# Kernel tuning notes

Hardware: AMD Instinct MI355X
Metric: run time of the kernel (lower is better)

## Reference

```python
import jax, jax.numpy as jnp
import numpy as np

HID = 4096; H = 128; P = 64; N = 128; G = 8; K = 4; CH = 128
INTER = H * P                      # 8192
CONV_DIM = INTER + 2 * G * N       # 10240
PROJ = INTER + CONV_DIM + H        # 18560
EPS = 1e-5


def segsum(x):
    # stable segment-sum: out[..., i, j] = sum_{j < k <= i} x[..., k]; -inf above diagonal
    T = x.shape[-1]
    xe = jnp.repeat(x[..., None], T, axis=-1)          # [..., i, j] = x[..., i]
    strict = jnp.tril(jnp.ones((T, T), bool), -1)
    s = jnp.cumsum(jnp.where(strict, xe, 0.0), axis=-2)
    keep = jnp.tril(jnp.ones((T, T), bool), 0)
    return jnp.where(keep, s, -jnp.inf)


def setup_inputs() -> dict:
    key = jax.random.key(0)
    ks = jax.random.split(key, 6)
    b, L = 2, 2048
    hidden_states = jax.random.normal(ks[0], (b, L, HID), jnp.float32)
    in_proj_w = jax.random.normal(ks[1], (PROJ, HID), jnp.float32) * (HID ** -0.5)
    conv_w = jax.random.normal(ks[2], (CONV_DIM, 1, K), jnp.float32) * 0.2
    conv_b = jax.random.normal(ks[3], (CONV_DIM,), jnp.float32) * 0.02
    dt_bias = jnp.ones((H,), jnp.float32)
    A_log = jnp.log(jnp.arange(1, H + 1, dtype=jnp.float32))
    D = jnp.ones((H,), jnp.float32)
    norm_weight = jnp.ones((INTER,), jnp.float32)
    out_proj_w = jax.random.normal(ks[4], (HID, INTER), jnp.float32) * (INTER ** -0.5)
    return dict(hidden_states=hidden_states, in_proj_w=in_proj_w, conv_w=conv_w, conv_b=conv_b,
                dt_bias=dt_bias, A_log=A_log, D=D, norm_weight=norm_weight, out_proj_w=out_proj_w)


def _mamba2(hidden_states, in_proj_w, conv_w, conv_b, dt_bias, A_log, D, norm_weight, out_proj_w):
    b, L, _ = hidden_states.shape
    nchunk = L // CH  # seq_len chosen to be a multiple of chunk_size (pad_size = 0)

    # in_proj and split into gate | conv path (x,B,C) | dt
    proj = hidden_states @ in_proj_w.T
    gate, hBC, dt = jnp.split(proj, [INTER, INTER + CONV_DIM], axis=-1)

    # causal depthwise conv1d (padding k-1, truncate) + SiLU
    xp = jnp.pad(hBC.transpose(0, 2, 1), ((0, 0), (0, 0), (K - 1, 0)))
    xc = jax.lax.conv_general_dilated(xp, conv_w, (1,), 'VALID',
                                      feature_group_count=CONV_DIM,
                                      dimension_numbers=('NCW', 'OIW', 'NCW'))
    hBC = jax.nn.silu((xc + conv_b[None, :, None]).transpose(0, 2, 1))
    hs, Bx, Cx = jnp.split(hBC, [INTER, INTER + G * N], axis=-1)

    A = -jnp.exp(A_log)                      # [H]
    dt = jax.nn.softplus(dt + dt_bias)       # time_step_limit = (0, inf) -> clamp is no-op

    hs = hs.reshape(b, L, H, P)
    rep = H // G
    Bm = jnp.tile(Bx.reshape(b, L, G, N), (1, 1, rep, 1))   # matches torch .repeat
    Cm = jnp.tile(Cx.reshape(b, L, G, N), (1, 1, rep, 1))

    D_res = D[None, None, :, None] * hs      # [b,L,H,P]

    # discretize and chunk
    X = (hs * dt[..., None]).reshape(b, nchunk, CH, H, P)
    A_dt = (A[None, None, :] * dt).reshape(b, nchunk, CH, H).transpose(0, 3, 1, 2)  # [b,H,c,l]
    Bc = Bm.reshape(b, nchunk, CH, H, N)
    Cc = Cm.reshape(b, nchunk, CH, H, N)
    A_cs = jnp.cumsum(A_dt, axis=-1)

    # 1. intra-chunk (diagonal blocks)
    Lmat = jnp.exp(segsum(A_dt))                              # [b,H,c,l,s]
    Gm = jnp.einsum('bclhn,bcshn->bclsh', Cc, Bc)
    M = Gm * Lmat.transpose(0, 2, 3, 4, 1)                    # [b,c,l,s,H]
    Y_diag = jnp.einsum('bclsh,bcshp->bclhp', M, X)

    # 2. per-chunk states
    decay_states = jnp.exp(A_cs[..., -1:] - A_cs)             # [b,H,c,l]
    B_decay = Bc * decay_states.transpose(0, 2, 3, 1)[..., None]
    states = jnp.einsum('bclhn,bclhp->bchpn', B_decay, X)     # [b,c,H,P,N]

    # 3. inter-chunk recurrence
    states = jnp.concatenate([jnp.zeros_like(states[:, :1]), states], axis=1)
    A_last = jnp.pad(A_cs[..., -1], ((0, 0), (0, 0), (1, 0)))  # [b,H,c+1]
    decay_chunk = jnp.exp(segsum(A_last)).transpose(0, 3, 2, 1)  # [b,c+1,c+1,H]
    new_states = jnp.einsum('bzjh,bzhpn->bjhpn', decay_chunk, states)
    prev_states = new_states[:, :-1]                           # [b,c,H,P,N]

    # 4. state -> output
    sdo = jnp.exp(A_cs).transpose(0, 2, 3, 1)                  # [b,c,l,H]
    Y_off = jnp.einsum('bclhn,bchpn->bclhp', Cc, prev_states) * sdo[..., None]

    y = (Y_diag + Y_off).reshape(b, L, H, P) + D_res
    scan_out = y.reshape(b, L, INTER)

    # gated group RMSNorm (norm_before_gate=False: gate first, then group-RMS)
    xg = scan_out * jax.nn.silu(gate)
    xr = xg.reshape(b, L, G, INTER // G)
    xr = xr * jax.lax.rsqrt(jnp.mean(xr * xr, axis=-1, keepdims=True) + EPS)
    normed = xr.reshape(b, L, INTER) * norm_weight

    return normed @ out_proj_w.T


def reference(hidden_states, in_proj_w, conv_w, conv_b, dt_bias, A_log, D, norm_weight, out_proj_w):
    return _mamba2(hidden_states, in_proj_w, conv_w, conv_b, dt_bias, A_log, D, norm_weight, out_proj_w)
```

## Files before the change

kernel.cpp:

```cpp
#include <hip/hip_runtime.h>

#define NH 128
#define PD 64
#define NSD 128
#define NG 8
#define CHK 128
#define HIDD 4096
#define INTER_D 8192
#define CONV_D 10240
#define PROJ_D 18560
#define SEQ 2048
#define ROWS 4096
#define NCH 16

typedef __attribute__((ext_vector_type(8))) short bf16x8;
typedef __attribute__((ext_vector_type(4))) float f32x4;

__device__ __forceinline__ unsigned short f2bf(float f) {
  unsigned int u = __float_as_uint(f);
  u += 0x7FFF + ((u >> 16) & 1);
  return (unsigned short)(u >> 16);
}
__device__ __forceinline__ float bf2f(unsigned short s) {
  return __uint_as_float(((unsigned int)s) << 16);
}

__device__ __forceinline__ void gld16(const unsigned short* g, unsigned short* l) {
  __builtin_amdgcn_global_load_lds(
      (__attribute__((address_space(1))) const void*)g,
      (__attribute__((address_space(3))) void*)l, 16, 0, 0);
}

#define BAR() __builtin_amdgcn_s_barrier()
#define SCHED() __builtin_amdgcn_sched_barrier(0)
#define VMCNT(n) asm volatile("s_waitcnt vmcnt(" #n ")" ::: "memory")

__device__ __forceinline__ bf16x8 ldsfrag(const unsigned short* slot, int row, int kslot) {
  int byte = row * 128 + (((kslot ^ (row & 7)) << 4));
  return *(const bf16x8*)((const char*)slot + byte);
}

__global__ __launch_bounds__(256) void cvt_all_kernel(const float* __restrict__ hs,
                                                      const float* __restrict__ w1,
                                                      const float* __restrict__ w2,
                                                      unsigned short* __restrict__ hsb,
                                                      unsigned short* __restrict__ w1b,
                                                      unsigned short* __restrict__ w2b) {
  int bid = blockIdx.x;
  const float* in;
  unsigned short* out;
  size_t base;
  if (bid < 16384) {
    in = hs; out = hsb; base = (size_t)bid * 1024;
  } else if (bid < 16384 + 74240) {
    in = w1; out = w1b; base = (size_t)(bid - 16384) * 1024;
  } else {
    in = w2; out = w2b; base = (size_t)(bid - 16384 - 74240) * 1024;
  }
  size_t i = base + (size_t)threadIdx.x * 4;
  float4 f = *(const float4*)(in + i);
  ushort4 o;
  o.x = f2bf(f.x); o.y = f2bf(f.y); o.z = f2bf(f.z); o.w = f2bf(f.w);
  *(ushort4*)(out + i) = o;
}

template <int OUT_BF16>
__global__ __launch_bounds__(512, 2) void gemm256(const unsigned short* __restrict__ A,
                                                  const unsigned short* __restrict__ B,
                                                  unsigned short* __restrict__ outb,
                                                  float* __restrict__ outf,
                                                  int Nreal, int Ks, int Kl, int koff) {
  __shared__ unsigned short lds[8][8192];
  int tid = threadIdx.x, l = tid & 63, w = tid >> 6;
  int wm = w >> 2, wn = w & 3;
  int il = l & 15, fog = l >> 4;
  int bid = blockIdx.x;
  int xcd = bid & 7, local = bid >> 3;
  int mt = xcd * 2 + (local & 1), nt = local >> 1;
  const unsigned short* Abase = A + (size_t)mt * 256 * Ks + koff;
  const unsigned short* Bbase = B + (size_t)nt * 256 * Ks + koff;
  int NT = Kl >> 6;

  f32x4 acc[2][2][4][2];
#pragma unroll
  for (int a = 0; a < 2; ++a)
#pragma unroll
    for (int b = 0; b < 2; ++b)
#pragma unroll
      for (int m = 0; m < 4; ++m)
#pragma unroll
        for (int n = 0; n < 2; ++n) acc[a][b][m][n] = (f32x4){0.f, 0.f, 0.f, 0.f};

  auto STG = [&](int tt, int ty) {
    int tc = tt < NT ? tt : NT - 1;
    const unsigned short* g = ((ty & 1) ? Bbase : Abase) + (size_t)((ty >> 1) * 128) * Ks + tc * 64;
    unsigned short* sp = (unsigned short*)lds[(tt & 1) * 4 + ty];
#pragma unroll
    for (int j = 0; j < 2; ++j) {
      int row = (j * 8 + w) * 8 + (l >> 3);
      int scol = ((l & 7) ^ (row & 7)) * 8;
      gld16(g + (size_t)row * Ks + scol, sp + (j * 8 + w) * 512);
    }
  };

#define LDA(SLOT)                                          \
  _Pragma("unroll") for (int mi = 0; mi < 4; ++mi)         \
  _Pragma("unroll") for (int kk = 0; kk < 2; ++kk)         \
      av[mi][kk] = ldsfrag(SLOT, wm * 64 + mi * 16 + il, kk * 4 + fog);
#define LDB(QN, SLOT)                                      \
  _Pragma("unroll") for (int ni = 0; ni < 2; ++ni)         \
  _Pragma("unroll") for (int kk = 0; kk < 2; ++kk)         \
      bv[QN][ni][kk] = ldsfrag(SLOT, wn * 32 + ni * 16 + il, kk * 4 + fog);
#define MFMA_PH(QM, QN)                                    \
  _Pragma("unroll") for (int mi = 0; mi < 4; ++mi)         \
  _Pragma("unroll") for (int ni = 0; ni < 2; ++ni)         \
  _Pragma("unroll") for (int kk = 0; kk < 2; ++kk)         \
      acc[QM][QN][mi][ni] = __builtin_amdgcn_mfma_f32_16x16x32_bf16( \
          av[mi][kk], bv[QN][ni][kk], acc[QM][QN][mi][ni], 0, 0, 0);

  STG(0, 0); STG(0, 1); STG(0, 3); STG(0, 2);
  VMCNT(2);
  BAR(); SCHED();

  for (int t = 0; t < NT; ++t) {
    const unsigned short* sA0 = lds[(t & 1) * 4 + 0];
    const unsigned short* sB0 = lds[(t & 1) * 4 + 1];
    const unsigned short* sA1 = lds[(t & 1) * 4 + 2];
    const unsigned short* sB1 = lds[(t & 1) * 4 + 3];
    bf16x8 av[4][2], bv[2][2][2];
    LDA(sA0); LDB(0, sB0); LDB(1, sB1);
    STG(t + 1, 0); STG(t + 1, 1);
    BAR();
    __builtin_amdgcn_s_setprio(1);
    MFMA_PH(0, 0);
    __builtin_amdgcn_s_setprio(0);
    VMCNT(4);
    BAR(); SCHED();
    STG(t + 1, 3);
    __builtin_amdgcn_s_setprio(1);
    MFMA_PH(0, 1);
    __builtin_amdgcn_s_setprio(0);
    BAR();
    LDA(sA1);
    STG(t + 1, 2);
    BAR();
    __builtin_amdgcn_s_setprio(1);
    MFMA_PH(1, 0);
    __builtin_amdgcn_s_setprio(0);
    BAR();
    __builtin_amdgcn_s_setprio(1);
    MFMA_PH(1, 1);
    __builtin_amdgcn_s_setprio(0);
    VMCNT(2);
    BAR(); SCHED();
  }
  VMCNT(0);

  int rl = (l >> 4) * 4;
#pragma unroll
  for (int qm = 0; qm < 2; ++qm)
#pragma unroll
    for (int qn = 0; qn < 2; ++qn)
#pragma unroll
      for (int mi = 0; mi < 4; ++mi)
#pragma unroll
        for (int ni = 0; ni < 2; ++ni) {
          int grow = mt * 256 + qm * 128 + wm * 64 + mi * 16 + rl;
          int gcol = nt * 256 + qn * 128 + wn * 32 + ni * 16 + il;
          if (!OUT_BF16 || gcol < Nreal) {
#pragma unroll
            for (int r = 0; r < 4; ++r) {
              float v = acc[qm][qn][mi][ni][r];
              if (OUT_BF16)
                outb[(size_t)(grow + r) * Nreal + gcol] = f2bf(v);
              else
                outf[(size_t)(grow + r) * Nreal + gcol] = v;
            }
          }
        }
#undef LDA
#undef LDB
#undef MFMA_PH
}

__global__ __launch_bounds__(256) void dtsa_kernel(const unsigned short* __restrict__ proj,
                                                   const float* __restrict__ dt_bias,
                                                   float* __restrict__ dtg) {
  int idx = blockIdx.x * 256 + threadIdx.x;
  int row = idx >> 7, h = idx & 127;
  float x = bf2f(proj[(size_t)row * PROJ_D + (PROJ_D - NH) + h]) + dt_bias[h];
  float d = (x > 20.f) ? x : log1pf(expf(x));
  dtg[(size_t)row * NH + h] = d;
}

__global__ __launch_bounds__(128) void dtsb_kernel(const float* __restrict__ dtg,
                                                   const float* __restrict__ A_log,
                                                   float* __restrict__ acsg) {
  int bc = blockIdx.x;
  int h = threadIdx.x;
  int b = bc >> 4, c = bc & 15;
  float A = -__expf(A_log[h]);
  float cum = 0.f;
  int row0 = b * SEQ + c * CHK;
#pragma unroll 8
  for (int ll = 0; ll < CHK; ++ll) {
    cum += A * dtg[(size_t)(row0 + ll) * NH + h];
    acsg[(((size_t)bc * NH) + h) * CHK + ll] = cum;
  }
}

__global__ __launch_bounds__(256) void conv_kernel(const unsigned short* __restrict__ proj,
                                                   const float* __restrict__ cw,
                                                   const float* __restrict__ cb,
                                                   unsigned short* __restrict__ xbc) {
  int ch0 = (blockIdx.x * 256 + threadIdx.x) * 8;
  int row = blockIdx.y;
  int b = row >> 11, ll = row & 2047;
  float4 cwv[8];
#pragma unroll
  for (int e = 0; e < 8; ++e) cwv[e] = *(const float4*)(cw + (ch0 + e) * 4);
  float acc[8];
#pragma unroll
  for (int e = 0; e < 8; ++e) acc[e] = cb[ch0 + e];
#pragma unroll
  for (int k = 0; k < 4; ++k) {
    int l2 = ll - 3 + k;
    if (l2 >= 0) {
      bf16x8 v = *(const bf16x8*)(proj + (size_t)(b * SEQ + l2) * PROJ_D + INTER_D + ch0);
#pragma unroll
      for (int e = 0; e < 8; ++e)
        acc[e] += bf2f(((unsigned short*)&v)[e]) * ((const float*)&cwv[e])[k];
    }
  }
  unsigned short o[8];
#pragma unroll
  for (int e = 0; e < 8; ++e) {
    float s = acc[e] / (1.f + __expf(-acc[e]));
    o[e] = f2bf(s);
  }
  *(int4*)(xbc + (size_t)row * CONV_D + ch0) = *(int4*)o;
}

__global__ __launch_bounds__(256) void e1b_kernel(const unsigned short* __restrict__ xbc,
                                                  const float* __restrict__ dtg,
                                                  const float* __restrict__ acsg,
                                                  unsigned short* __restrict__ states16) {
  int bid = blockIdx.x;
  int h = bid & 127, c = (bid >> 7) & 15, b = bid >> 11;
  int g = h & 7;
  int row0 = b * SEQ + c * CHK;
  __shared__ __align__(16) char smem[52736];
  unsigned short* XT = (unsigned short*)smem;
  unsigned short* BdT = (unsigned short*)(smem + 17408);
  float* Acs = (float*)(smem + 52224);
  int tid = threadIdx.x, lane = tid & 63, wv = tid >> 6;
  int fo = (lane >> 4) * 8, il = lane & 15, rl = (lane >> 4) * 4;
  if (tid < 128) Acs[tid] = acsg[(((size_t)(b * NCH + c) * NH) + h) * CHK + tid];
  __syncthreads();
#pragma unroll
  for (int j = 0; j < 4; ++j) {
    int q = tid + j * 256;
    int ll = q >> 3, p0 = (q & 7) * 8;
    int row = row0 + ll;
    float dtv = dtg[(size_t)row * NH + h];
    int4 raw = *(const int4*)(xbc + (size_t)row * CONV_D + h * PD + p0);
    unsigned short* u = (unsigned short*)&raw;
#pragma unroll
    for (int e = 0; e < 8; ++e) XT[(p0 + e) * 136 + ll] = f2bf(bf2f(u[e]) * dtv);
  }
#pragma unroll
  for (int j = 0; j < 8; ++j) {
    int q = tid + j * 256;
    int ll = q >> 4, n0 = (q & 15) * 8;
    float dec = __expf(Acs[CHK - 1] - Acs[ll]);
    int4 raw = *(const int4*)(xbc + (size_t)(row0 + ll) * CONV_D + INTER_D + g * NSD + n0);
    unsigned short* u = (unsigned short*)&raw;
#pragma unroll
    for (int e = 0; e < 8; ++e) BdT[(n0 + e) * 136 + ll] = f2bf(bf2f(u[e]) * dec);
  }
  __syncthreads();
  f32x4 st[8];
#pragma unroll
  for (int i = 0; i < 8; ++i) st[i] = (f32x4){0.f, 0.f, 0.f, 0.f};
#pragma unroll
  for (int ks = 0; ks < 4; ++ks) {
    bf16x8 a = *(const bf16x8*)&XT[(wv * 16 + il) * 136 + ks * 32 + fo];
#pragma unroll
    for (int ni = 0; ni < 8; ++ni) {
      bf16x8 bb = *(const bf16x8*)&BdT[(ni * 16 + il) * 136 + ks * 32 + fo];
      st[ni] = __builtin_amdgcn_mfma_f32_16x16x32_bf16(a, bb, st[ni], 0, 0, 0);
    }
  }
  size_t base = ((size_t)(b * NH + h) * NCH + c) * (PD * NSD);
#pragma unroll
  for (int ni = 0; ni < 8; ++ni) {
    int n = ni * 16 + il;
#pragma unroll
    for (int r = 0; r < 4; ++r) {
      int p = wv * 16 + rl + r;
      states16[base + p * NSD + n] = f2bf(st[ni][r]);
    }
  }
}

__global__ __launch_bounds__(256) void e2_kernel(const float* __restrict__ acsg,
                                                 const unsigned short* __restrict__ states16,
                                                 unsigned short* __restrict__ prevs) {
  int bid = blockIdx.x;
  int bh = bid >> 2, pg = bid & 3;
  int b = bh >> 7;
  int t = threadIdx.x;
  float S[8];
#pragma unroll
  for (int j = 0; j < 8; ++j) S[j] = 0.f;
  for (int c = 0; c < NCH; ++c) {
    float alast = acsg[(((size_t)((b * NCH + c) * NH) + (bh & 127))) * CHK + (CHK - 1)];
    float dec = __expf(alast);
    size_t base = ((size_t)bh * NCH + c) * (PD * NSD) + (size_t)pg * 2048 + (size_t)t * 8;
    bf16x8 v = *(const bf16x8*)(states16 + base);
    unsigned short o[8];
#pragma unroll
    for (int j = 0; j < 8; ++j) {
      o[j] = f2bf(S[j]);
      S[j] = S[j] * dec + bf2f(((unsigned short*)&v)[j]);
    }
    *(bf16x8*)(prevs + base) = *(bf16x8*)o;
  }
}

__global__ __launch_bounds__(512) void e13_kernel(const unsigned short* __restrict__ xbc,
                                                  const float* __restrict__ dtg,
                                                  const float* __restrict__ acsg,
                                                  const unsigned short* __restrict__ prevs,
                                                  const float* __restrict__ Dp,
                                                  unsigned short* __restrict__ ybh) {
  int bid = blockIdx.x;
  int h = bid & 127, c = (bid >> 7) & 15, b = bid >> 11;
  int g = h & 7;
  int row0 = b * SEQ + c * CHK;
  __shared__ __align__(16) char smem[70144];
  unsigned short* Cst = (unsigned short*)smem;
  unsigned short* Bst = (unsigned short*)(smem + 10240);
  unsigned short* Mt = (unsigned short*)smem;
  unsigned short* XT = (unsigned short*)(smem + 34816);
  unsigned short* Sp = (unsigned short*)(smem + 52224);
  float* Acs = (float*)(smem + 69632);
  int tid = threadIdx.x, lane = tid & 63, wv = tid >> 6;
  int fo = (lane >> 4) * 8, il = lane & 15, rl = (lane >> 4) * 4;
  if (tid < 128) Acs[tid] = acsg[(((size_t)(b * NCH + c) * NH) + h) * CHK + tid];

  f32x4 gm[8];
#pragma unroll
  for (int i = 0; i < 8; ++i) gm[i] = (f32x4){0.f, 0.f, 0.f, 0.f};
  bf16x8 cf[4];
  int srow = tid >> 2, scol = (tid & 3) * 8;
#pragma unroll
  for (int kc = 0; kc < 4; ++kc) {
    __syncthreads();
    *(int4*)(Cst + srow * 40 + scol) =
        *(const int4*)(xbc + (size_t)(row0 + srow) * CONV_D + INTER_D + NG * NSD + g * NSD + kc * 32 + scol);
    *(int4*)(Bst + srow * 40 + scol) =
        *(const int4*)(xbc + (size_t)(row0 + srow) * CONV_D + INTER_D + g * NSD + kc * 32 + scol);
    __syncthreads();
    bf16x8 a = *(const bf16x8*)&Cst[(wv * 16 + il) * 40 + fo];
    cf[kc] = a;
#pragma unroll
    for (int ni = 0; ni < 8; ++ni) {
      bf16x8 bb = *(const bf16x8*)&Bst[(ni * 16 + il) * 40 + fo];
      gm[ni] = __builtin_amdgcn_mfma_f32_16x16x32_bf16(a, bb, gm[ni], 0, 0, 0);
    }
  }
  __syncthreads();
#pragma unroll
  for (int ni = 0; ni < 8; ++ni) {
    int s = ni * 16 + il;
#pragma unroll
    for (int r = 0; r < 4; ++r) {
      int ll = wv * 16 + rl + r;
      float v = (s <= ll) ? gm[ni][r] * __expf(Acs[ll] - Acs[s]) : 0.f;
      Mt[ll * 136 + s] = f2bf(v);
    }
  }
#pragma unroll
  for (int j = 0; j < 2; ++j) {
    int q = tid + j * 512;
    int ll = q >> 3, p0 = (q & 7) * 8;
    int row = row0 + ll;
    float dtv = dtg[(size_t)row * NH + h];
    int4 raw = *(const int4*)(xbc + (size_t)row * CONV_D + h * PD + p0);
    unsigned short* u = (unsigned short*)&raw;
#pragma unroll
    for (int e = 0; e < 8; ++e) XT[(p0 + e) * 136 + ll] = f2bf(bf2f(u[e]) * dtv);
  }
  size_t sbase = ((size_t)(b * NH + h) * NCH + c) * (PD * NSD);
#pragma unroll
  for (int j = 0; j < 2; ++j) {
    int q = tid + j * 512;
    int p = q >> 4, n0 = (q & 15) * 8;
    *(int4*)(Sp + p * 136 + n0) = *(const int4*)(prevs + sbase + p * NSD + n0);
  }
  __syncthreads();
  f32x4 yd[4], yo[4];
#pragma unroll
  for (int i = 0; i < 4; ++i) {
    yd[i] = (f32x4){0.f, 0.f, 0.f, 0.f};
    yo[i] = (f32x4){0.f, 0.f, 0.f, 0.f};
  }
#pragma unroll
  for (int ks = 0; ks < 4; ++ks) {
    bf16x8 a = *(const bf16x8*)&Mt[(wv * 16 + il) * 136 + ks * 32 + fo];
#pragma unroll
    for (int pi = 0; pi < 4; ++pi) {
      bf16x8 bb = *(const bf16x8*)&XT[(pi * 16 + il) * 136 + ks * 32 + fo];
      bf16x8 sb = *(const bf16x8*)&Sp[(pi * 16 + il) * 136 + ks * 32 + fo];
      yd[pi] = __builtin_amdgcn_mfma_f32_16x16x32_bf16(a, bb, yd[pi], 0, 0, 0);
      yo[pi] = __builtin_amdgcn_mfma_f32_16x16x32_bf16(cf[ks], sb, yo[pi], 0, 0, 0);
    }
  }
  float dv = Dp[h];
#pragma unroll
  for (int pi = 0; pi < 4; ++pi) {
    int p = pi * 16 + il;
#pragma unroll
    for (int r = 0; r < 4; ++r) {
      int ll = wv * 16 + rl + r;
      int row = row0 + ll;
      float hsv = bf2f(xbc[(size_t)row * CONV_D + h * PD + p]);
      ybh[(size_t)row * INTER_D + h * PD + p] =
          f2bf(yd[pi][r] + yo[pi][r] * __expf(Acs[ll]) + dv * hsv);
    }
  }
}

__global__ __launch_bounds__(256) void fnorm_kernel(const unsigned short* __restrict__ ybh,
                                                    const unsigned short* __restrict__ proj,
                                                    const float* __restrict__ nw,
                                                    unsigned short* __restrict__ normed) {
  int gid = blockIdx.x * 4 + (threadIdx.x >> 6);
  int lane = threadIdx.x & 63;
  int row = gid >> 3, gg = gid & 7;
  int ch = gg * 1024 + lane * 16;
  bf16x8 y0 = *(const bf16x8*)(ybh + (size_t)row * INTER_D + ch);
  bf16x8 y1 = *(const bf16x8*)(ybh + (size_t)row * INTER_D + ch + 8);
  bf16x8 g0 = *(const bf16x8*)(proj + (size_t)row * PROJ_D + ch);
  bf16x8 g1 = *(const bf16x8*)(proj + (size_t)row * PROJ_D + ch + 8);
  float v[16];
  float ss = 0.f;
#pragma unroll
  for (int j = 0; j < 8; ++j) {
    float val = bf2f(((unsigned short*)&y0)[j]);
    float gt = bf2f(((unsigned short*)&g0)[j]);
    val *= gt / (1.f + __expf(-gt));
    v[j] = val; ss += val * val;
  }
#pragma unroll
  for (int j = 0; j < 8; ++j) {
    float val = bf2f(((unsigned short*)&y1)[j]);
    float gt = bf2f(((unsigned short*)&g1)[j]);
    val *= gt / (1.f + __expf(-gt));
    v[8 + j] = val; ss += val * val;
  }
#pragma unroll
  for (int o = 1; o < 64; o <<= 1) ss += __shfl_xor(ss, o, 64);
  float rms = rsqrtf(ss / 1024.f + 1e-5f);
  unsigned short o16[16];
#pragma unroll
  for (int q = 0; q < 4; ++q) {
    float4 nwv = *(const float4*)(nw + ch + q * 4);
    const float* nwp = (const float*)&nwv;
#pragma unroll
    for (int j = 0; j < 4; ++j) o16[q * 4 + j] = f2bf(v[q * 4 + j] * rms * nwp[j]);
  }
  *(int4*)(normed + (size_t)row * INTER_D + ch) = *(int4*)o16;
  *(int4*)(normed + (size_t)row * INTER_D + ch + 8) = *(int4*)(o16 + 8);
}

extern "C" void kernel_launch(void* const* d_in, const int* in_sizes, int n_in,
                              void* d_out, int out_size, void* d_ws, size_t ws_size,
                              hipStream_t stream) {
  (void)in_sizes; (void)n_in; (void)out_size; (void)ws_size;
  const float* hs = (const float*)d_in[0];
  const float* w1 = (const float*)d_in[1];
  const float* cw = (const float*)d_in[2];
  const float* cb = (const float*)d_in[3];
  const float* dtb = (const float*)d_in[4];
  const float* alog = (const float*)d_in[5];
  const float* Dp = (const float*)d_in[6];
  const float* nw = (const float*)d_in[7];
  const float* w2 = (const float*)d_in[8];
  float* out = (float*)d_out;
  char* ws = (char*)d_ws;

  unsigned short* hsb = (unsigned short*)(ws);
  unsigned short* w1b = (unsigned short*)(ws + 33554432);
  unsigned short* w2b = (unsigned short*)(ws + 186646528);
  unsigned short* proj = (unsigned short*)(ws + 253755392);
  unsigned short* xbc = (unsigned short*)(ws + 405798912);
  float* dtg = (float*)(ws + 489684992);
  float* acsg = (float*)(ws + 491782144);
  unsigned short* states16 = (unsigned short*)(ws + 493879296);
  unsigned short* prevs = (unsigned short*)(ws + 560988160);
  unsigned short* ybh = (unsigned short*)(ws + 628097024);
  unsigned short* normed = (unsigned short*)(ws);

  cvt_all_kernel<<<dim3(123392), dim3(256), 0, stream>>>(hs, w1, w2, hsb, w1b, w2b);

  gemm256<1><<<dim3(16 * 73), dim3(512), 0, stream>>>(hsb, w1b, proj, nullptr,
                                                      PROJ_D, HIDD, HIDD, 0);
  dtsa_kernel<<<dim3(2048), dim3(256), 0, stream>>>(proj, dtb, dtg);
  dtsb_kernel<<<dim3(32), dim3(128), 0, stream>>>(dtg, alog, acsg);
  conv_kernel<<<dim3(5, 4096), dim3(256), 0, stream>>>(proj, cw, cb, xbc);
  e1b_kernel<<<dim3(4096), dim3(256), 0, stream>>>(xbc, dtg, acsg, states16);
  e2_kernel<<<dim3(1024), dim3(256), 0, stream>>>(acsg, states16, prevs);
  e13_kernel<<<dim3(4096), dim3(512), 0, stream>>>(xbc, dtg, acsg, prevs, Dp, ybh);
  fnorm_kernel<<<dim3(8192), dim3(256), 0, stream>>>(ybh, proj, nw, normed);
  gemm256<0><<<dim3(16 * 16), dim3(512), 0, stream>>>(normed, w2b, nullptr, out,
                                                      HIDD, INTER_D, INTER_D, 0);
}
```

Measured before the change: 1.313 ms.

## Deepen GEMM prefetch pipeline to two tiles ahead with explicit LDS waits

```diff
diff --git a/kernel.cpp b/kernel.cpp
--- a/kernel.cpp
+++ b/kernel.cpp
@@ -31,9 +31,15 @@
       (__attribute__((address_space(3))) void*)l, 16, 0, 0);
 }
 
-#define BAR() __builtin_amdgcn_s_barrier()
 #define SCHED() __builtin_amdgcn_sched_barrier(0)
 #define VMCNT(n) asm volatile("s_waitcnt vmcnt(" #n ")" ::: "memory")
+#define LGKM(n) asm volatile("s_waitcnt lgkmcnt(" #n ")" ::: "memory")
+#define BARF()                              \
+  do {                                      \
+    asm volatile("" ::: "memory");          \
+    __builtin_amdgcn_s_barrier();           \
+    asm volatile("" ::: "memory");          \
+  } while (0)
 
 __device__ __forceinline__ bf16x8 ldsfrag(const unsigned short* slot, int row, int kslot) {
   int byte = row * 128 + (((kslot ^ (row & 7)) << 4));
@@ -107,52 +113,66 @@
   _Pragma("unroll") for (int mi = 0; mi < 4; ++mi)         \
   _Pragma("unroll") for (int kk = 0; kk < 2; ++kk)         \
       av[mi][kk] = ldsfrag(SLOT, wm * 64 + mi * 16 + il, kk * 4 + fog);
-#define LDB(QN, SLOT)                                      \
+#define LDBQ(DST, SLOT)                                    \
   _Pragma("unroll") for (int ni = 0; ni < 2; ++ni)         \
   _Pragma("unroll") for (int kk = 0; kk < 2; ++kk)         \
-      bv[QN][ni][kk] = ldsfrag(SLOT, wn * 32 + ni * 16 + il, kk * 4 + fog);
-#define MFMA_PH(QM, QN)                                    \
+      DST[ni][kk] = ldsfrag(SLOT, wn * 32 + ni * 16 + il, kk * 4 + fog);
+#define MFMA_PH(QM, QN, BV)                                \
   _Pragma("unroll") for (int mi = 0; mi < 4; ++mi)         \
   _Pragma("unroll") for (int ni = 0; ni < 2; ++ni)         \
   _Pragma("unroll") for (int kk = 0; kk < 2; ++kk)         \
       acc[QM][QN][mi][ni] = __builtin_amdgcn_mfma_f32_16x16x32_bf16( \
-          av[mi][kk], bv[QN][ni][kk], acc[QM][QN][mi][ni], 0, 0, 0);
+          av[mi][kk], BV[ni][kk], acc[QM][QN][mi][ni], 0, 0, 0);
+
+#define PH_TILE(BI, T)                                                       \
+  {                                                                          \
+    const unsigned short* sA0 = lds[(BI) * 4 + 0];                           \
+    const unsigned short* sB0 = lds[(BI) * 4 + 1];                           \
+    const unsigned short* sA1 = lds[(BI) * 4 + 2];                           \
+    const unsigned short* sB1 = lds[(BI) * 4 + 3];                           \
+    bf16x8 av[4][2], bv0[2][2], bv1[2][2];                                   \
+     \
+    LDA(sA0); LDBQ(bv0, sB0); LDBQ(bv1, sB1);                                \
+    STG((T) + 1, 2);                                                         \
+    LGKM(8);                                                                 \
+    BARF();                                                                  \
+    LGKM(0); SCHED();                                                        \
+    __builtin_amdgcn_s_setprio(1); MFMA_PH(0, 0, bv0);                       \
+    __builtin_amdgcn_s_setprio(0);                                           \
+    BARF();                                                                  \
+             \
+    STG((T) + 2, 0);                                                         \
+    BARF();                                                                  \
+    SCHED();                                                                 \
+    __builtin_amdgcn_s_setprio(1); MFMA_PH(0, 1, bv1);                       \
+    __builtin_amdgcn_s_setprio(0);                                           \
+    BARF();                                                                  \
+           \
+    LDA(sA1);                                                                \
+    STG((T) + 2, 1);                                                         \
+    BARF();                                                                  \
+    LGKM(0); SCHED();                                                        \
+    __builtin_amdgcn_s_setprio(1); MFMA_PH(1, 0, bv0);                       \
+    __builtin_amdgcn_s_setprio(0);                                           \
+    BARF();                                                                  \
+       \
+    STG((T) + 2, 3);                                                         \
+    BARF();                                                                  \
+    SCHED();                                                                 \
+    __builtin_amdgcn_s_setprio(1); MFMA_PH(1, 1, bv1);                       \
+    __builtin_amdgcn_s_setprio(0);                                           \
+    VMCNT(6);                                                                \
+    BARF();                                                                  \
+  }
 
   STG(0, 0); STG(0, 1); STG(0, 3); STG(0, 2);
-  VMCNT(2);
-  BAR(); SCHED();
-
-  for (int t = 0; t < NT; ++t) {
-    const unsigned short* sA0 = lds[(t & 1) * 4 + 0];
-    const unsigned short* sB0 = lds[(t & 1) * 4 + 1];
-    const unsigned short* sA1 = lds[(t & 1) * 4 + 2];
-    const unsigned short* sB1 = lds[(t & 1) * 4 + 3];
-    bf16x8 av[4][2], bv[2][2][2];
-    LDA(sA0); LDB(0, sB0); LDB(1, sB1);
-    STG(t + 1, 0); STG(t + 1, 1);
-    BAR();
-    __builtin_amdgcn_s_setprio(1);
-    MFMA_PH(0, 0);
-    __builtin_amdgcn_s_setprio(0);
-    VMCNT(4);
-    BAR(); SCHED();
-    STG(t + 1, 3);
-    __builtin_amdgcn_s_setprio(1);
-    MFMA_PH(0, 1);
-    __builtin_amdgcn_s_setprio(0);
-    BAR();
-    LDA(sA1);
-    STG(t + 1, 2);
-    BAR();
-    __builtin_amdgcn_s_setprio(1);
-    MFMA_PH(1, 0);
-    __builtin_amdgcn_s_setprio(0);
-    BAR();
-    __builtin_amdgcn_s_setprio(1);
-    MFMA_PH(1, 1);
-    __builtin_amdgcn_s_setprio(0);
-    VMCNT(2);
-    BAR(); SCHED();
+  STG(1, 0); STG(1, 1); STG(1, 3);
+  VMCNT(6);
+  BARF(); SCHED();
+
+  for (int t = 0; t < NT; t += 2) {
+    PH_TILE(0, t);
+    PH_TILE(1, t + 1);
   }
   VMCNT(0);
 
@@ -179,8 +199,9 @@
           }
         }
 #undef LDA
-#undef LDB
+#undef LDBQ
 #undef MFMA_PH
+#undef PH_TILE
 }
 
 __global__ __launch_bounds__(256) void dtsa_kernel(const unsigned short* __restrict__ proj,
```

New measurement: 1.292 ms. No clear change (-1.6%).
